# Performance work log

Measured on AMD Instinct MI355X. Metric: run time of the kernel, lower is better.

The kernel has to match this reference:

```python
import jax, jax.numpy as jnp
import numpy as np

BLOCK = 64      # base classifier input height/width
STRIDE = 16     # BLOCK // 4 per Windowing(stride=[1,bh/4,bw/4,1], size=[1,bh,bw,1])
K = 10          # n_classes
THRESH = 0.7    # bbox_threshold


def extract_patches(x):
    # x: [B,H,W,C] -> [B,R,Cc,BLOCK*BLOCK*C], same layout as tf.image.extract_patches
    B, H, Wd, C = x.shape
    R = (H - BLOCK) // STRIDE + 1
    Cc = (Wd - BLOCK) // STRIDE + 1
    rows = jnp.arange(R)[:, None] * STRIDE + jnp.arange(BLOCK)[None, :]   # [R,64]
    cols = jnp.arange(Cc)[:, None] * STRIDE + jnp.arange(BLOCK)[None, :]  # [Cc,64]
    p = x[:, rows]                 # [B,R,64,W,C]
    p = p[:, :, :, cols]           # [B,R,64,Cc,64,C]
    p = jnp.transpose(p, (0, 1, 3, 2, 4, 5))  # [B,R,Cc,64,64,C]
    return p.reshape(B, R, Cc, BLOCK * BLOCK * C)


def connected_components(mask):
    # 4-connected components of a 2D bool mask via iterative min-label propagation.
    # Background = 0; foreground labels are distinct positive ints per component.
    R, C = mask.shape
    big = jnp.int32(R * C + 2)
    init = jnp.where(mask, jnp.arange(1, R * C + 1, dtype=jnp.int32).reshape(R, C), 0)

    def step(lab, _):
        l = jnp.where(mask, lab, big)
        up = jnp.concatenate([jnp.full((1, C), big, l.dtype), l[:-1]], 0)
        dn = jnp.concatenate([l[1:], jnp.full((1, C), big, l.dtype)], 0)
        lf = jnp.concatenate([jnp.full((R, 1), big, l.dtype), l[:, :-1]], 1)
        rt = jnp.concatenate([l[:, 1:], jnp.full((R, 1), big, l.dtype)], 1)
        m = jnp.minimum(jnp.minimum(l, jnp.minimum(up, dn)), jnp.minimum(lf, rt))
        return jnp.where(mask, m, 0), None

    lab, _ = jax.lax.scan(step, init, None, length=2 * (R + C))
    return lab


def boxes_from_labels(lab):
    # Segmented min/max over label ids replaces the per-region python loop:
    # box = [rowmin-1, colmin-1, rowmax+1, colmax+1] per component.
    R, C = lab.shape
    N = R * C
    flat = lab.reshape(N)
    rr = jnp.arange(N, dtype=jnp.int32) // C
    cc = jnp.arange(N, dtype=jnp.int32) % C
    rmin = jax.ops.segment_min(rr, flat, num_segments=N + 1)
    cmin = jax.ops.segment_min(cc, flat, num_segments=N + 1)
    rmax = jax.ops.segment_max(rr, flat, num_segments=N + 1)
    cmax = jax.ops.segment_max(cc, flat, num_segments=N + 1)
    cnt = jax.ops.segment_sum(jnp.ones(N, jnp.int32), flat, num_segments=N + 1)
    valid = (cnt > 0).at[0].set(False)  # slot 0 is background
    boxes = jnp.stack([rmin - 1, cmin - 1, rmax + 1, cmax + 1], -1)
    boxes = jnp.where(valid[:, None], boxes, 0)
    return boxes, valid


def setup_inputs() -> dict:
    key = jax.random.key(0)
    k1, k2, k3 = jax.random.split(key, 3)
    inputs = jax.random.normal(k1, (1, 1024, 1024, 3), dtype=jnp.float32)
    # scale W so logits have ~unit variance -> sparse (realistic) threshold mask
    W = jax.random.normal(k2, (12288, K), dtype=jnp.float32) * 0.01
    b = jax.random.normal(k3, (K,), dtype=jnp.float32)
    return {"inputs": inputs, "W": W, "b": b}


def reference(inputs, W, b):
    patches = extract_patches(inputs)               # [1,R,Cc,D]
    B, R, Cc, D = patches.shape
    logits = patches.reshape(B * R * Cc, D) @ W + b # [N,K]
    prob = jax.nn.softmax(logits, axis=1).reshape(R, Cc, K)
    mask = prob > THRESH                            # [R,Cc,K]
    labels = jax.vmap(connected_components, in_axes=2, out_axes=2)(mask)  # [R,Cc,K]
    boxes, valid = jax.vmap(boxes_from_labels)(jnp.transpose(labels, (2, 0, 1)))
    # boxes: [K, R*Cc+1, 4] padded per-component bboxes; valid: [K, R*Cc+1]
    return prob, labels, boxes, valid
```

## Files before the change

kernel.cpp:

```cpp
#include <hip/hip_runtime.h>
#include <cmath>

#define KCLS 10
#define NCELL 3721
#define BIGV  0x0FFFFFFF

#define OUT_PROB 0
#define OUT_LAB  37210
#define OUT_BOX  74420
#define OUT_VALID 223300

#define DPPADD(x, ctrl) \
    x += __int_as_float(__builtin_amdgcn_update_dpp( \
        0, __float_as_int(x), ctrl, 0xf, 0xf, true))

__device__ __forceinline__ float wave_sum64(float x) {
    DPPADD(x, 0x111);
    DPPADD(x, 0x112);
    DPPADD(x, 0x114);
    DPPADD(x, 0x118);
    DPPADD(x, 0x142);
    DPPADD(x, 0x143);
    return x;
}

__device__ __forceinline__ int swz_fidx(int j) {
    const int row = j / 10;
    const int c   = j - row * 10;
    return (row << 4) + (((c >> 2) ^ ((row >> 1) & 3)) << 2) + (c & 3);
}

__global__ __launch_bounds__(512, 4) void k1_logits(
    const float* __restrict__ x, const float* __restrict__ W,
    const float* __restrict__ b, float* __restrict__ out)
{
    const int tid  = threadIdx.x;
    const int tsub = tid & 255;
    const int kh   = tid >> 8;
    const int r    = blockIdx.x >> 3;
    const int cg   = blockIdx.x & 7;
    const int c0   = (cg == 7) ? 53 : cg * 8;

    __shared__ float  wbuf[2][256 * 16];
    __shared__ float  red[8][8][5];
    __shared__ double lgs[8][KCLS];

    const int j0 = tid << 2;
    const int d0 = swz_fidx(j0);
    const int d1 = swz_fidx(j0 + 2);
    const int je = 2048 + tid;
    const int d2 = swz_fidx(je);

    const int s3 = (tsub >> 1) & 3;
    const int rb = tsub << 4;
    const int q0 = rb + ((0 ^ s3) << 2);
    const int q1 = rb + ((1 ^ s3) << 2);
    const int q2 = rb + ((2 ^ s3) << 2);

    int i   = (tsub >= 192) ? 1 : 0;
    int rem = tsub - i * 192;
    const float* xb = x + r * 49152 + c0 * 48;

    float acc[8][5];
#pragma unroll
    for (int p = 0; p < 8; ++p)
#pragma unroll
        for (int k = 0; k < 5; ++k) acc[p][k] = 0.0f;

    float4 sv; float s1;
    {
        const float4 v0 = *(const float4*)(W + j0);
        const float  v1 = W[je];
        float* wb0 = &wbuf[0][0];
        *(float2*)(wb0 + d0) = make_float2(v0.x, v0.y);
        *(float2*)(wb0 + d1) = make_float2(v0.z, v0.w);
        wb0[d2] = v1;
        const float* ws = W + 2560;
        sv = *(const float4*)(ws + j0);
        s1 = ws[je];
    }

    for (int it = 0; it < 48; ++it) {
        __syncthreads();
        if (it + 1 < 48) {
            float* wbn = &wbuf[(it + 1) & 1][0];
            *(float2*)(wbn + d0) = make_float2(sv.x, sv.y);
            *(float2*)(wbn + d1) = make_float2(sv.z, sv.w);
            wbn[d2] = s1;
            if (it + 2 < 48) {
                const float* ws = W + (it + 2) * 2560;
                sv = *(const float4*)(ws + j0);
                s1 = ws[je];
            }
        }
        const float* xp = xb + i * 3072 + rem;
        float xv[8];
#pragma unroll
        for (int p = 0; p < 8; ++p) xv[p] = xp[p * 48];

        const float* wb = &wbuf[it & 1][0];
        float wv[5];
        if (kh == 0) {
            const float4 a = *(const float4*)(wb + q0);
            wv[0] = a.x; wv[1] = a.y; wv[2] = a.z; wv[3] = a.w;
            wv[4] = wb[q1];
        } else {
            const float4 a = *(const float4*)(wb + q1);
            const float2 c = *(const float2*)(wb + q2);
            wv[0] = a.y; wv[1] = a.z; wv[2] = a.w; wv[3] = c.x; wv[4] = c.y;
        }
#pragma unroll
        for (int p = 0; p < 8; ++p)
#pragma unroll
            for (int k = 0; k < 5; ++k) acc[p][k] += xv[p] * wv[k];

        rem += 64; ++i;
        if (rem >= 192) { rem -= 192; ++i; }
    }

    const int w = tid >> 6;
#pragma unroll
    for (int p = 0; p < 8; ++p)
#pragma unroll
        for (int k = 0; k < 5; ++k) {
            const float s = wave_sum64(acc[p][k]);
            if ((tid & 63) == 63) red[w][p][k] = s;
        }
    __syncthreads();

    if (tid < 80) {
        const int p  = tid / 10;
        const int kk = tid - p * 10;
        const int khk = (kk >= 5) ? 1 : 0;
        const int k5  = kk - khk * 5;
        double s = (double)b[kk];
#pragma unroll
        for (int j = 0; j < 4; ++j) s += (double)red[khk * 4 + j][p][k5];
        lgs[p][kk] = s;
    }
    __syncthreads();

    if (tid < 8) {
        const int cc = c0 + tid;
        double l[KCLS];
#pragma unroll
        for (int k = 0; k < KCLS; ++k) l[k] = lgs[tid][k];
        double m = l[0];
#pragma unroll
        for (int k = 1; k < KCLS; ++k) m = fmax(m, l[k]);
        double e[KCLS], ssum = 0.0;
#pragma unroll
        for (int k = 0; k < KCLS; ++k) { e[k] = exp(l[k] - m); ssum += e[k]; }
        const double inv = 1.0 / ssum;
        float* po = out + OUT_PROB + (size_t)(r * 61 + cc) * KCLS;
#pragma unroll
        for (int k = 0; k < KCLS; ++k) po[k] = (float)(e[k] * inv);
    }
}

__global__ __launch_bounds__(1024) void k2_cc_boxes(float* __restrict__ out)
{
    const int k   = blockIdx.x;
    const int tid = threadIdx.x;

    __shared__ int lab[63 * 64];
    __shared__ int act[NCELL];
    __shared__ int nact, changed;
    __shared__ int rmn[NCELL + 1], rmx[NCELL + 1], cmn[NCELL + 1], cmx[NCELL + 1];

    for (int idx = tid; idx < 63 * 64; idx += 1024) lab[idx] = BIGV;
    for (int s = tid; s <= NCELL; s += 1024) {
        rmn[s] = 0x7fffffff; cmn[s] = 0x7fffffff; rmx[s] = -1; cmx[s] = -1;
    }
    if (tid == 0) nact = 0;
    __syncthreads();

    for (int idx = tid; idx < NCELL; idx += 1024) {
        const float pv = out[OUT_PROB + (size_t)idx * KCLS + k];
        if (pv > 0.7f) {
            const int r = idx / 61, c = idx - r * 61;
            const int off = (r + 1) * 64 + (c + 1);
            lab[off] = off;
            act[atomicAdd(&nact, 1)] = off;
        }
    }
    __syncthreads();
    const int na = nact;

    for (int round = 0; round < 128; ++round) {
        if (tid == 0) changed = 0;
        __syncthreads();
        bool ch = false;
        for (int ii = tid; ii < na; ii += 1024) {
            const int off = act[ii];
            const int v = lab[off];
            int m = v, t;
            t = lab[off - 1];  if (t < m) m = t;
            t = lab[off + 1];  if (t < m) m = t;
            t = lab[off - 64]; if (t < m) m = t;
            t = lab[off + 64]; if (t < m) m = t;
            if (m < v) {
                int p = lab[m];
                while (p < m) { m = p; p = lab[m]; }
                atomicMin(&lab[off], m);
                atomicMin(&lab[v],   m);
                ch = true;
            }
        }
        if (ch) changed = 1;
        __syncthreads();
        if (changed == 0) break;
        __syncthreads();
    }

    for (int idx = tid; idx < NCELL; idx += 1024) {
        const int r = idx / 61, c = idx - r * 61;
        const int v = lab[(r + 1) * 64 + (c + 1)];
        const int lv = (v < BIGV) ? ((v >> 6) * 61 - 61 + (v & 63)) : 0;
        out[OUT_LAB + (size_t)idx * KCLS + k] = (float)lv;
    }

    for (int ii = tid; ii < na; ii += 1024) {
        const int off = act[ii];
        const int v = lab[off];
        const int lb = (v >> 6) * 61 - 61 + (v & 63);
        const int r = (off >> 6) - 1, c = (off & 63) - 1;
        atomicMin(&rmn[lb], r); atomicMax(&rmx[lb], r);
        atomicMin(&cmn[lb], c); atomicMax(&cmx[lb], c);
    }
    __syncthreads();

    for (int s = tid; s <= NCELL; s += 1024) {
        const bool val = (s > 0) && (rmx[s] >= 0);
        float* bo = out + OUT_BOX + (size_t)(k * (NCELL + 1) + s) * 4;
        if (val) {
            bo[0] = (float)(rmn[s] - 1);
            bo[1] = (float)(cmn[s] - 1);
            bo[2] = (float)(rmx[s] + 1);
            bo[3] = (float)(cmx[s] + 1);
        } else {
            bo[0] = 0.0f; bo[1] = 0.0f; bo[2] = 0.0f; bo[3] = 0.0f;
        }
        out[OUT_VALID + (size_t)k * (NCELL + 1) + s] = val ? 1.0f : 0.0f;
    }
}

extern "C" void kernel_launch(void* const* d_in, const int* in_sizes, int n_in,
                              void* d_out, int out_size, void* d_ws, size_t ws_size,
                              hipStream_t stream) {
    const float* x = (const float*)d_in[0];
    const float* W = (const float*)d_in[1];
    const float* b = (const float*)d_in[2];
    float* out = (float*)d_out;

    k1_logits  <<<dim3(488), dim3(512), 0, stream>>>(x, W, b, out);
    k2_cc_boxes<<<dim3(KCLS), dim3(1024), 0, stream>>>(out);
}
```

Baseline: 101.5 us.

## Split logits into split-K partial kernel plus separate reduce-softmax kernel

Replaces the single logits kernel with a split-K scheme. 1952 blocks each stage two input image rows in LDS and compute partial dot products for all 61 columns of a patch row over a 384-wide slice of the reduction, reading W directly from global memory. A second kernel sums the 32 partials in double precision, adds the bias and applies softmax. This raises parallelism and reuses each staged input row across overlapping patches. The cost is an extra launch and a workspace round trip for the partials.

Result: faster. 93.76 us (-7.6%).

```diff
diff --git a/kernel.cpp b/kernel.cpp
--- a/kernel.cpp
+++ b/kernel.cpp
@@ -10,138 +10,100 @@
 #define OUT_BOX  74420
 #define OUT_VALID 223300
 
-#define DPPADD(x, ctrl) \
-    x += __int_as_float(__builtin_amdgcn_update_dpp( \
-        0, __float_as_int(x), ctrl, 0xf, 0xf, true))
-
-__device__ __forceinline__ float wave_sum64(float x) {
-    DPPADD(x, 0x111);
-    DPPADD(x, 0x112);
-    DPPADD(x, 0x114);
-    DPPADD(x, 0x118);
-    DPPADD(x, 0x142);
-    DPPADD(x, 0x143);
-    return x;
-}
-
-__device__ __forceinline__ int swz_fidx(int j) {
-    const int row = j / 10;
-    const int c   = j - row * 10;
-    return (row << 4) + (((c >> 2) ^ ((row >> 1) & 3)) << 2) + (c & 3);
-}
-
-__global__ __launch_bounds__(512, 4) void k1_logits(
+#define XROW_PAD 3328
+
+#define WF(q, n) ( ((n)&3)==0 ? (q)[(n)>>2].x : ((n)&3)==1 ? (q)[(n)>>2].y : \
+                   ((n)&3)==2 ? (q)[(n)>>2].z : (q)[(n)>>2].w )
+
+__global__ __launch_bounds__(256, 4) void k1a_partial(
     const float* __restrict__ x, const float* __restrict__ W,
-    const float* __restrict__ b, float* __restrict__ out)
+    float* __restrict__ partial)
 {
     const int tid  = threadIdx.x;
-    const int tsub = tid & 255;
-    const int kh   = tid >> 8;
-    const int r    = blockIdx.x >> 3;
-    const int cg   = blockIdx.x & 7;
-    const int c0   = (cg == 7) ? 53 : cg * 8;
-
-    __shared__ float  wbuf[2][256 * 16];
-    __shared__ float  red[8][8][5];
-    __shared__ double lgs[8][KCLS];
-
-    const int j0 = tid << 2;
-    const int d0 = swz_fidx(j0);
-    const int d1 = swz_fidx(j0 + 2);
-    const int je = 2048 + tid;
-    const int d2 = swz_fidx(je);
-
-    const int s3 = (tsub >> 1) & 3;
-    const int rb = tsub << 4;
-    const int q0 = rb + ((0 ^ s3) << 2);
-    const int q1 = rb + ((1 ^ s3) << 2);
-    const int q2 = rb + ((2 ^ s3) << 2);
-
-    int i   = (tsub >= 192) ? 1 : 0;
-    int rem = tsub - i * 192;
-    const float* xb = x + r * 49152 + c0 * 48;
-
-    float acc[8][5];
-#pragma unroll
-    for (int p = 0; p < 8; ++p)
-#pragma unroll
-        for (int k = 0; k < 5; ++k) acc[p][k] = 0.0f;
-
-    float4 sv; float s1;
-    {
-        const float4 v0 = *(const float4*)(W + j0);
-        const float  v1 = W[je];
-        float* wb0 = &wbuf[0][0];
-        *(float2*)(wb0 + d0) = make_float2(v0.x, v0.y);
-        *(float2*)(wb0 + d1) = make_float2(v0.z, v0.w);
-        wb0[d2] = v1;
-        const float* ws = W + 2560;
-        sv = *(const float4*)(ws + j0);
-        s1 = ws[je];
-    }
-
-    for (int it = 0; it < 48; ++it) {
-        __syncthreads();
-        if (it + 1 < 48) {
-            float* wbn = &wbuf[(it + 1) & 1][0];
-            *(float2*)(wbn + d0) = make_float2(sv.x, sv.y);
-            *(float2*)(wbn + d1) = make_float2(sv.z, sv.w);
-            wbn[d2] = s1;
-            if (it + 2 < 48) {
-                const float* ws = W + (it + 2) * 2560;
-                sv = *(const float4*)(ws + j0);
-                s1 = ws[je];
+    const int bid  = blockIdx.x;
+    const int i2   = bid / 61;
+    const int r    = bid - i2 * 61;
+    const int lane = tid & 63;
+    const int tq   = tid >> 6;
+    const int tqu  = __builtin_amdgcn_readfirstlane(tq);
+    const int cc   = (lane < 61) ? lane : 60;
+
+    __shared__ float xrow[2][XROW_PAD];
+    __shared__ float red[4][61][KCLS];
+
+#pragma unroll
+    for (int ii = 0; ii < 2; ++ii) {
+        const float* g = x + (size_t)((r << 4) + (i2 << 1) + ii) * 3072;
+#pragma unroll
+        for (int j = 0; j < 3; ++j) {
+            const int idx = tid + (j << 8);
+            const float4 v = *(const float4*)(g + (idx << 2));
+            const int p = idx << 2;
+            float* d = &xrow[ii][p + ((p / 48) << 2)];
+            d[0] = v.x; d[1] = v.y; d[2] = v.z; d[3] = v.w;
+        }
+    }
+    __syncthreads();
+
+    float acc[KCLS];
+#pragma unroll
+    for (int k = 0; k < KCLS; ++k) acc[k] = 0.0f;
+
+#pragma unroll
+    for (int ii = 0; ii < 2; ++ii) {
+        const int dbase = ((i2 << 1) + ii) * 192 + tqu * 48;
+        const float* wrow = W + (size_t)dbase * KCLS;
+        const float* lrow = &xrow[ii][52 * (cc + tqu)];
+#pragma unroll
+        for (int u = 0; u < 12; ++u) {
+            const float4 xv = *(const float4*)(lrow + (u << 2));
+            const float* wp = wrow + 40 * u;
+            float4 wq[10];
+#pragma unroll
+            for (int j = 0; j < 10; ++j) wq[j] = *(const float4*)(wp + (j << 2));
+#pragma unroll
+            for (int k = 0; k < KCLS; ++k) {
+                acc[k] += xv.x * WF(wq, k);
+                acc[k] += xv.y * WF(wq, 10 + k);
+                acc[k] += xv.z * WF(wq, 20 + k);
+                acc[k] += xv.w * WF(wq, 30 + k);
             }
         }
-        const float* xp = xb + i * 3072 + rem;
-        float xv[8];
-#pragma unroll
-        for (int p = 0; p < 8; ++p) xv[p] = xp[p * 48];
-
-        const float* wb = &wbuf[it & 1][0];
-        float wv[5];
-        if (kh == 0) {
-            const float4 a = *(const float4*)(wb + q0);
-            wv[0] = a.x; wv[1] = a.y; wv[2] = a.z; wv[3] = a.w;
-            wv[4] = wb[q1];
-        } else {
-            const float4 a = *(const float4*)(wb + q1);
-            const float2 c = *(const float2*)(wb + q2);
-            wv[0] = a.y; wv[1] = a.z; wv[2] = a.w; wv[3] = c.x; wv[4] = c.y;
-        }
-#pragma unroll
-        for (int p = 0; p < 8; ++p)
-#pragma unroll
-            for (int k = 0; k < 5; ++k) acc[p][k] += xv[p] * wv[k];
-
-        rem += 64; ++i;
-        if (rem >= 192) { rem -= 192; ++i; }
-    }
-
-    const int w = tid >> 6;
-#pragma unroll
-    for (int p = 0; p < 8; ++p)
-#pragma unroll
-        for (int k = 0; k < 5; ++k) {
-            const float s = wave_sum64(acc[p][k]);
-            if ((tid & 63) == 63) red[w][p][k] = s;
-        }
-    __syncthreads();
-
-    if (tid < 80) {
-        const int p  = tid / 10;
-        const int kk = tid - p * 10;
-        const int khk = (kk >= 5) ? 1 : 0;
-        const int k5  = kk - khk * 5;
-        double s = (double)b[kk];
-#pragma unroll
-        for (int j = 0; j < 4; ++j) s += (double)red[khk * 4 + j][p][k5];
-        lgs[p][kk] = s;
-    }
-    __syncthreads();
-
-    if (tid < 8) {
-        const int cc = c0 + tid;
+    }
+
+    if (lane < 61) {
+#pragma unroll
+        for (int k = 0; k < KCLS; ++k) red[tq][lane][k] = acc[k];
+    }
+    __syncthreads();
+
+    for (int t = tid; t < 610; t += 256) {
+        const int c = t / 10, k = t - c * 10;
+        const float s = red[0][c][k] + red[1][c][k] + red[2][c][k] + red[3][c][k];
+        partial[(size_t)i2 * 37210 + (size_t)r * 610 + (size_t)c * 10 + k] = s;
+    }
+}
+
+__global__ __launch_bounds__(640) void k1b_softmax(
+    const float* __restrict__ partial, const float* __restrict__ b,
+    float* __restrict__ out)
+{
+    const int r   = blockIdx.x;
+    const int tid = threadIdx.x;
+    __shared__ double lgs[61][KCLS];
+
+    if (tid < 610) {
+        const int c = tid / 10, k = tid - c * 10;
+        double s = (double)b[k];
+        const float* p = partial + (size_t)r * 610 + tid;
+#pragma unroll 8
+        for (int i2 = 0; i2 < 32; ++i2)
+            s += (double)p[(size_t)i2 * 37210];
+        lgs[c][k] = s;
+    }
+    __syncthreads();
+
+    if (tid < 61) {
         double l[KCLS];
 #pragma unroll
         for (int k = 0; k < KCLS; ++k) l[k] = lgs[tid][k];
@@ -152,7 +114,7 @@
 #pragma unroll
         for (int k = 0; k < KCLS; ++k) { e[k] = exp(l[k] - m); ssum += e[k]; }
         const double inv = 1.0 / ssum;
-        float* po = out + OUT_PROB + (size_t)(r * 61 + cc) * KCLS;
+        float* po = out + OUT_PROB + (size_t)(r * 61 + tid) * KCLS;
 #pragma unroll
         for (int k = 0; k < KCLS; ++k) po[k] = (float)(e[k] * inv);
     }
@@ -251,8 +213,10 @@
     const float* x = (const float*)d_in[0];
     const float* W = (const float*)d_in[1];
     const float* b = (const float*)d_in[2];
-    float* out = (float*)d_out;
-
-    k1_logits  <<<dim3(488), dim3(512), 0, stream>>>(x, W, b, out);
+    float* out     = (float*)d_out;
+    float* partial = (float*)d_ws;
+
+    k1a_partial<<<dim3(1952), dim3(256), 0, stream>>>(x, W, partial);
+    k1b_softmax<<<dim3(61),   dim3(640), 0, stream>>>(partial, b, out);
     k2_cc_boxes<<<dim3(KCLS), dim3(1024), 0, stream>>>(out);
 }
```

## Transpose W in a pre-pass and read it directly from global memory in logits

Applied to the files above, without the earlier changes.

Adds a small kernel that transposes W into a class-major layout in workspace. The logits kernel then drops the shared-memory double-buffered W staging and its per-iteration barriers. Each thread instead loads float2 pairs of all 10 class weights straight from global/L2 and accumulates all classes itself, reducing across 8 waves at the end. This removes LDS traffic and syncs, at the cost of an extra launch, more registers (80 accumulators) and repeated global W reads across 488 blocks.

After: 114.7 us. 1.13x slower.

```diff
diff --git a/kernel.cpp b/kernel.cpp
--- a/kernel.cpp
+++ b/kernel.cpp
@@ -24,127 +24,91 @@
     return x;
 }
 
-__device__ __forceinline__ int swz_fidx(int j) {
-    const int row = j / 10;
-    const int c   = j - row * 10;
-    return (row << 4) + (((c >> 2) ^ ((row >> 1) & 3)) << 2) + (c & 3);
-}
-
-__global__ __launch_bounds__(512, 4) void k1_logits(
-    const float* __restrict__ x, const float* __restrict__ W,
+__global__ __launch_bounds__(256) void k0_transpose(
+    const float* __restrict__ W, float* __restrict__ WT)
+{
+    const int d = blockIdx.x * 256 + threadIdx.x;
+    const float2 a0 = *(const float2*)(W + (size_t)d * KCLS + 0);
+    const float2 a1 = *(const float2*)(W + (size_t)d * KCLS + 2);
+    const float2 a2 = *(const float2*)(W + (size_t)d * KCLS + 4);
+    const float2 a3 = *(const float2*)(W + (size_t)d * KCLS + 6);
+    const float2 a4 = *(const float2*)(W + (size_t)d * KCLS + 8);
+    WT[0 * 12288 + d] = a0.x;  WT[1 * 12288 + d] = a0.y;
+    WT[2 * 12288 + d] = a1.x;  WT[3 * 12288 + d] = a1.y;
+    WT[4 * 12288 + d] = a2.x;  WT[5 * 12288 + d] = a2.y;
+    WT[6 * 12288 + d] = a3.x;  WT[7 * 12288 + d] = a3.y;
+    WT[8 * 12288 + d] = a4.x;  WT[9 * 12288 + d] = a4.y;
+}
+
+__global__ __launch_bounds__(512, 4) void k1a_logits(
+    const float* __restrict__ x, const float* __restrict__ WT,
     const float* __restrict__ b, float* __restrict__ out)
 {
-    const int tid  = threadIdx.x;
-    const int tsub = tid & 255;
-    const int kh   = tid >> 8;
-    const int r    = blockIdx.x >> 3;
-    const int cg   = blockIdx.x & 7;
-    const int c0   = (cg == 7) ? 53 : cg * 8;
-
-    __shared__ float  wbuf[2][256 * 16];
-    __shared__ float  red[8][8][5];
-    __shared__ double lgs[8][KCLS];
-
-    const int j0 = tid << 2;
-    const int d0 = swz_fidx(j0);
-    const int d1 = swz_fidx(j0 + 2);
-    const int je = 2048 + tid;
-    const int d2 = swz_fidx(je);
-
-    const int s3 = (tsub >> 1) & 3;
-    const int rb = tsub << 4;
-    const int q0 = rb + ((0 ^ s3) << 2);
-    const int q1 = rb + ((1 ^ s3) << 2);
-    const int q2 = rb + ((2 ^ s3) << 2);
-
-    int i   = (tsub >= 192) ? 1 : 0;
-    int rem = tsub - i * 192;
-    const float* xb = x + r * 49152 + c0 * 48;
-
-    float acc[8][5];
+    const int tid = threadIdx.x;
+    const int r   = blockIdx.x >> 3;
+    const int cg  = blockIdx.x & 7;
+    const int c0  = (cg == 7) ? 53 : cg * 8;
+    __shared__ float red[8][8][KCLS];
+
+    float acc[8][KCLS];
 #pragma unroll
     for (int p = 0; p < 8; ++p)
 #pragma unroll
-        for (int k = 0; k < 5; ++k) acc[p][k] = 0.0f;
-
-    float4 sv; float s1;
-    {
-        const float4 v0 = *(const float4*)(W + j0);
-        const float  v1 = W[je];
-        float* wb0 = &wbuf[0][0];
-        *(float2*)(wb0 + d0) = make_float2(v0.x, v0.y);
-        *(float2*)(wb0 + d1) = make_float2(v0.z, v0.w);
-        wb0[d2] = v1;
-        const float* ws = W + 2560;
-        sv = *(const float4*)(ws + j0);
-        s1 = ws[je];
-    }
-
-    for (int it = 0; it < 48; ++it) {
-        __syncthreads();
-        if (it + 1 < 48) {
-            float* wbn = &wbuf[(it + 1) & 1][0];
-            *(float2*)(wbn + d0) = make_float2(sv.x, sv.y);
-            *(float2*)(wbn + d1) = make_float2(sv.z, sv.w);
-            wbn[d2] = s1;
-            if (it + 2 < 48) {
-                const float* ws = W + (it + 2) * 2560;
-                sv = *(const float4*)(ws + j0);
-                s1 = ws[je];
-            }
-        }
-        const float* xp = xb + i * 3072 + rem;
-        float xv[8];
-#pragma unroll
-        for (int p = 0; p < 8; ++p) xv[p] = xp[p * 48];
-
-        const float* wb = &wbuf[it & 1][0];
-        float wv[5];
-        if (kh == 0) {
-            const float4 a = *(const float4*)(wb + q0);
-            wv[0] = a.x; wv[1] = a.y; wv[2] = a.z; wv[3] = a.w;
-            wv[4] = wb[q1];
-        } else {
-            const float4 a = *(const float4*)(wb + q1);
-            const float2 c = *(const float2*)(wb + q2);
-            wv[0] = a.y; wv[1] = a.z; wv[2] = a.w; wv[3] = c.x; wv[4] = c.y;
-        }
-#pragma unroll
-        for (int p = 0; p < 8; ++p)
-#pragma unroll
-            for (int k = 0; k < 5; ++k) acc[p][k] += xv[p] * wv[k];
-
-        rem += 64; ++i;
-        if (rem >= 192) { rem -= 192; ++i; }
+        for (int k = 0; k < KCLS; ++k) acc[p][k] = 0.0f;
+
+    int i = (2 * tid) / 192;
+    int t = (2 * tid) - i * 192;
+    const float* wtb = WT + 2 * tid;
+
+    for (int u = 0; u < 12; ++u) {
+        const float* xb = x + (size_t)(r * 16 + i) * 3072 + 48 * c0 + t;
+        const float* wb = wtb + (u << 10);
+
+        float2 wt[KCLS];
+#pragma unroll
+        for (int k = 0; k < KCLS; ++k) wt[k] = *(const float2*)(wb + 12288 * k);
+
+        float2 xv[4];
+#pragma unroll
+        for (int p = 0; p < 4; ++p) xv[p] = *(const float2*)(xb + 48 * p);
+#pragma unroll
+        for (int p = 0; p < 4; ++p)
+#pragma unroll
+            for (int k = 0; k < KCLS; ++k)
+                acc[p][k] += xv[p].x * wt[k].x + xv[p].y * wt[k].y;
+
+#pragma unroll
+        for (int p = 0; p < 4; ++p) xv[p] = *(const float2*)(xb + 192 + 48 * p);
+#pragma unroll
+        for (int p = 0; p < 4; ++p)
+#pragma unroll
+            for (int k = 0; k < KCLS; ++k)
+                acc[4 + p][k] += xv[p].x * wt[k].x + xv[p].y * wt[k].y;
+
+        t += 64; i += 5;
+        if (t >= 192) { t -= 192; ++i; }
     }
 
     const int w = tid >> 6;
 #pragma unroll
     for (int p = 0; p < 8; ++p)
 #pragma unroll
-        for (int k = 0; k < 5; ++k) {
+        for (int k = 0; k < KCLS; ++k) {
             const float s = wave_sum64(acc[p][k]);
             if ((tid & 63) == 63) red[w][p][k] = s;
         }
-    __syncthreads();
-
-    if (tid < 80) {
-        const int p  = tid / 10;
-        const int kk = tid - p * 10;
-        const int khk = (kk >= 5) ? 1 : 0;
-        const int k5  = kk - khk * 5;
-        double s = (double)b[kk];
-#pragma unroll
-        for (int j = 0; j < 4; ++j) s += (double)red[khk * 4 + j][p][k5];
-        lgs[p][kk] = s;
-    }
     __syncthreads();
 
     if (tid < 8) {
         const int cc = c0 + tid;
         double l[KCLS];
 #pragma unroll
-        for (int k = 0; k < KCLS; ++k) l[k] = lgs[tid][k];
+        for (int k = 0; k < KCLS; ++k) {
+            double s = (double)b[k];
+#pragma unroll
+            for (int w2 = 0; w2 < 8; ++w2) s += (double)red[w2][tid][k];
+            l[k] = s;
+        }
         double m = l[0];
 #pragma unroll
         for (int k = 1; k < KCLS; ++k) m = fmax(m, l[k]);
@@ -252,7 +216,9 @@
     const float* W = (const float*)d_in[1];
     const float* b = (const float*)d_in[2];
     float* out = (float*)d_out;
-
-    k1_logits  <<<dim3(488), dim3(512), 0, stream>>>(x, W, b, out);
-    k2_cc_boxes<<<dim3(KCLS), dim3(1024), 0, stream>>>(out);
-}
+    float* WT  = (float*)d_ws;
+
+    k0_transpose<<<dim3(48),  dim3(256),  0, stream>>>(W, WT);
+    k1a_logits  <<<dim3(488), dim3(512),  0, stream>>>(x, WT, b, out);
+    k2_cc_boxes <<<dim3(KCLS), dim3(1024), 0, stream>>>(out);
+}
```
